# Kernel tuning notes

Measured on AMD Instinct MI355X. Metric: run time of the kernel, lower is better.

## Reference

```python
import jax, jax.numpy as jnp
import numpy as np

TEMPERATURE = 8.0  # sqrt(d_k), d_k = 64


def setup_inputs() -> dict:
    key = jax.random.key(0)
    kq, kk, kv, km = jax.random.split(key, 4)
    B, Lq, Lk, D = 64, 1024, 1024, 64
    q = jax.random.normal(kq, (B, Lq, D), dtype=jnp.float32)
    k = jax.random.normal(kk, (B, Lk, D), dtype=jnp.float32)
    v = jax.random.normal(kv, (B, Lk, D), dtype=jnp.float32)
    mask = jax.random.randint(km, (B, Lq, Lk), 0, 2).astype(jnp.bool_)
    return {"q": q, "k": k, "v": v, "mask": mask}


def reference(q, k, v, mask):
    # attn = q @ k^T / temperature, masked softmax over last dim, then @ v
    attn = jnp.einsum("bqd,bkd->bqk", q, k) / TEMPERATURE
    attn = jnp.where(mask, -jnp.inf, attn)
    attn = jax.nn.softmax(attn, axis=2)
    output = jnp.einsum("bqk,bkd->bqd", attn, v)
    return (output, attn)
```

## Files before the change

kernel.cpp:

```cpp
#include <hip/hip_runtime.h>
#include <hip/hip_bf16.h>


typedef __attribute__((ext_vector_type(8))) short bf16x8;
typedef __attribute__((ext_vector_type(4))) short bf16x4;
typedef __attribute__((ext_vector_type(4))) float f32x4;

#define GLOBAL_AS __attribute__((address_space(1)))
#define LDS_AS    __attribute__((address_space(3)))

static __device__ __forceinline__ short f2bf(float f) {
    return (short)__builtin_bit_cast(unsigned short, __float2bfloat16(f));
}
static __device__ __forceinline__ bf16x8 pack8(float4 a, float4 b) {
    union { bf16x8 v; __hip_bfloat162 h[4]; } u;
    u.h[0] = __float22bfloat162_rn(make_float2(a.x, a.y));
    u.h[1] = __float22bfloat162_rn(make_float2(a.z, a.w));
    u.h[2] = __float22bfloat162_rn(make_float2(b.x, b.y));
    u.h[3] = __float22bfloat162_rn(make_float2(b.z, b.w));
    return u.v;
}
static __device__ __forceinline__ bf16x4 pack4(float a, float b, float c, float d) {
    union { bf16x4 v; __hip_bfloat162 h[2]; } u;
    u.h[0] = __float22bfloat162_rn(make_float2(a, b));
    u.h[1] = __float22bfloat162_rn(make_float2(c, d));
    return u.v;
}

static __device__ __forceinline__ void dma16(void* lds, const void* g) {
    __builtin_amdgcn_global_load_lds((const GLOBAL_AS unsigned*)g,
                                     (LDS_AS unsigned*)lds, 16, 0, 0);
}
static __device__ __forceinline__ void stage8k(short* lds, const short* g, int w, int L) {
    dma16((void*)(lds + (w * 2 + 0) * 512), (const void*)(g + (w * 2 + 0) * 512 + L * 8));
    dma16((void*)(lds + (w * 2 + 1) * 512), (const void*)(g + (w * 2 + 1) * 512 + L * 8));
}

__global__ __launch_bounds__(256) void pre_maskpack(const int* __restrict__ mask,
                                                    unsigned long long* __restrict__ bits) {
    const int L = threadIdx.x & 63;
    long r = ((long)blockIdx.x * 256 + threadIdx.x) >> 6;
    const int* row = mask + r * 1024;
    unsigned long long bl[16];
    #pragma unroll
    for (int kt = 0; kt < 16; ++kt)
        bl[kt] = __ballot(row[kt * 64 + L] != 0);
    unsigned long long x = bl[0];
    #pragma unroll
    for (int j = 1; j < 16; ++j) x = (L == j) ? bl[j] : x;
    if (L < 16) bits[r * 16 + L] = x;
}

__global__ __launch_bounds__(256) void pre_kv(const float* __restrict__ k,
                                              const float* __restrict__ v,
                                              short* __restrict__ kb,
                                              short* __restrict__ vt) {
    __shared__ short t[64][72];
    const int tid = threadIdx.x;
    if (blockIdx.x < 2048) {
        long ci = (long)blockIdx.x * 256 + tid;
        long row = ci >> 3;
        int  c   = (int)(ci & 7);
        const float4* s = (const float4*)(k + row * 64 + c * 8);
        int r = (int)(row & 63);
        short* dst = kb + (row >> 6) * 4096 + (long)r * 64 + ((c ^ (r & 7)) << 3);
        *(bf16x8*)dst = pack8(s[0], s[1]);
    } else {
        const int bkt = blockIdx.x - 2048;
        const int row = tid >> 2;
        const int cg  = (tid & 3) * 16;
        const float* src = v + ((long)bkt * 64 + row) * 64 + cg;
        float4 f0 = ((const float4*)src)[0];
        float4 f1 = ((const float4*)src)[1];
        float4 f2 = ((const float4*)src)[2];
        float4 f3 = ((const float4*)src)[3];
        float vv[16] = {f0.x, f0.y, f0.z, f0.w, f1.x, f1.y, f1.z, f1.w,
                        f2.x, f2.y, f2.z, f2.w, f3.x, f3.y, f3.z, f3.w};
        #pragma unroll
        for (int dd = 0; dd < 16; ++dd) t[cg + dd][row] = f2bf(vv[dd]);
        __syncthreads();
        const int d = tid >> 2, c0 = (tid & 3) * 2;
        short* dstrow = vt + (long)bkt * 4096 + d * 64;
        *(int4*)&dstrow[((c0 ^ (d & 7)) << 3)]       = *(int4*)&t[d][c0 * 8];
        *(int4*)&dstrow[(((c0 + 1) ^ (d & 7)) << 3)] = *(int4*)&t[d][c0 * 8 + 8];
    }
}

__global__ __launch_bounds__(256, 4) void attn_main(
    const float* __restrict__ q, const unsigned long long* __restrict__ bits,
    const short* __restrict__ kb, const short* __restrict__ vt,
    float* __restrict__ out, float* __restrict__ attn)
{
    __shared__ short kbuf[2][4096];
    __shared__ short vbuf[2][4096];
    __shared__ short ptile[4][1024];

    const int tid  = threadIdx.x;
    const int w    = tid >> 6;
    const int L    = tid & 63;
    const int n    = L & 15;
    const int g    = L >> 4;
    const int b    = blockIdx.y;
    const long bq  = (long)b * 1024 + blockIdx.x * 64;

    const short* ktg = kb + (long)b * 65536;
    const short* vtg = vt + (long)b * 65536;

    const float* qrow = q + (bq + 16 * w + n) * 64 + g * 8;
    float4 qa0 = ((const float4*)qrow)[0];
    float4 qa1 = ((const float4*)(qrow + 4))[0];
    float4 qb0 = ((const float4*)(qrow + 32))[0];
    float4 qb1 = ((const float4*)(qrow + 36))[0];
    const float sc = 0.125f * 1.4426950408889634f;
    qa0.x *= sc; qa0.y *= sc; qa0.z *= sc; qa0.w *= sc;
    qa1.x *= sc; qa1.y *= sc; qa1.z *= sc; qa1.w *= sc;
    qb0.x *= sc; qb0.y *= sc; qb0.z *= sc; qb0.w *= sc;
    qb1.x *= sc; qb1.y *= sc; qb1.z *= sc; qb1.w *= sc;
    bf16x8 qf0 = pack8(qa0, qa1);
    bf16x8 qf1 = pack8(qb0, qb1);

    const unsigned long long* mrow_ptr = bits + (bq + 16 * w + n) * 16;
    const int sw = (n & 7);

    float lp = 0.f;
    stage8k(kbuf[0], ktg, w, L);
    __syncthreads();

    for (int kt = 0; kt < 16; ++kt) {
        if (kt < 15) {
            stage8k(kbuf[(kt + 1) & 1], ktg + (kt + 1) * 4096, w, L);
        } else {
            stage8k(kbuf[0], ktg, w, L);
            stage8k(vbuf[0], vtg, w, L);
        }
        unsigned long long mrow = mrow_ptr[kt];
        const short* kl = kbuf[kt & 1];
        f32x4 acc[4];
        #pragma unroll
        for (int t = 0; t < 4; ++t) { acc[t][0]=0.f; acc[t][1]=0.f; acc[t][2]=0.f; acc[t][3]=0.f; }
        #pragma unroll
        for (int t = 0; t < 4; ++t) {
            bf16x8 kf0 = *(const bf16x8*)&kl[(t * 16 + n) * 64 + ((g ^ sw) << 3)];
            bf16x8 kf1 = *(const bf16x8*)&kl[(t * 16 + n) * 64 + (((4 + g) ^ sw) << 3)];
            acc[t] = __builtin_amdgcn_mfma_f32_16x16x32_bf16(kf0, qf0, acc[t], 0, 0, 0);
            acc[t] = __builtin_amdgcn_mfma_f32_16x16x32_bf16(kf1, qf1, acc[t], 0, 0, 0);
        }
        unsigned long long ms = mrow >> (g * 4);
        #pragma unroll
        for (int t = 0; t < 4; ++t)
            #pragma unroll
            for (int i = 0; i < 4; ++i) {
                unsigned bit = (unsigned)(ms >> (t * 16 + i)) & 1u;
                lp += bit ? 0.f : __builtin_exp2f(acc[t][i]);
            }
        __syncthreads();
    }
    float l = lp + __shfl_xor(lp, 16);
    l += __shfl_xor(l, 32);
    const float linv = 1.0f / l;

    f32x4 oacc[4];
    #pragma unroll
    for (int u = 0; u < 4; ++u) { oacc[u][0]=0.f; oacc[u][1]=0.f; oacc[u][2]=0.f; oacc[u][3]=0.f; }

    float* attn_row = attn + (bq + 16 * w + n) * 1024;
    short* pw = ptile[w];

    for (int kt = 0; kt < 16; ++kt) {
        if (kt < 15) {
            stage8k(kbuf[(kt + 1) & 1], ktg + (kt + 1) * 4096, w, L);
            stage8k(vbuf[(kt + 1) & 1], vtg + (kt + 1) * 4096, w, L);
        }
        unsigned long long mrow = mrow_ptr[kt];
        const short* kl = kbuf[kt & 1];
        const short* vl = vbuf[kt & 1];
        f32x4 acc[4];
        #pragma unroll
        for (int t = 0; t < 4; ++t) { acc[t][0]=0.f; acc[t][1]=0.f; acc[t][2]=0.f; acc[t][3]=0.f; }
        #pragma unroll
        for (int t = 0; t < 4; ++t) {
            bf16x8 kf0 = *(const bf16x8*)&kl[(t * 16 + n) * 64 + ((g ^ sw) << 3)];
            bf16x8 kf1 = *(const bf16x8*)&kl[(t * 16 + n) * 64 + (((4 + g) ^ sw) << 3)];
            acc[t] = __builtin_amdgcn_mfma_f32_16x16x32_bf16(kf0, qf0, acc[t], 0, 0, 0);
            acc[t] = __builtin_amdgcn_mfma_f32_16x16x32_bf16(kf1, qf1, acc[t], 0, 0, 0);
        }
        unsigned long long ms = mrow >> (g * 4);
        #pragma unroll
        for (int t = 0; t < 4; ++t) {
            unsigned b0 = (unsigned)(ms >> (t * 16 + 0)) & 1u;
            unsigned b1 = (unsigned)(ms >> (t * 16 + 1)) & 1u;
            unsigned b2 = (unsigned)(ms >> (t * 16 + 2)) & 1u;
            unsigned b3 = (unsigned)(ms >> (t * 16 + 3)) & 1u;
            float p0 = b0 ? 0.f : __builtin_exp2f(acc[t][0]) * linv;
            float p1 = b1 ? 0.f : __builtin_exp2f(acc[t][1]) * linv;
            float p2 = b2 ? 0.f : __builtin_exp2f(acc[t][2]) * linv;
            float p3 = b3 ? 0.f : __builtin_exp2f(acc[t][3]) * linv;
            *(float4*)(attn_row + kt * 64 + t * 16 + g * 4) = make_float4(p0, p1, p2, p3);
            *(bf16x4*)&pw[n * 64 + ((((t * 2) + (g >> 1)) ^ sw) << 3) + (g & 1) * 4] =
                pack4(p0, p1, p2, p3);
        }
        bf16x8 pf0 = *(const bf16x8*)&pw[n * 64 + ((g ^ sw) << 3)];
        bf16x8 pf1 = *(const bf16x8*)&pw[n * 64 + (((4 + g) ^ sw) << 3)];
        #pragma unroll
        for (int u = 0; u < 4; ++u) {
            bf16x8 vf0 = *(const bf16x8*)&vl[(u * 16 + n) * 64 + ((g ^ sw) << 3)];
            bf16x8 vf1 = *(const bf16x8*)&vl[(u * 16 + n) * 64 + (((4 + g) ^ sw) << 3)];
            oacc[u] = __builtin_amdgcn_mfma_f32_16x16x32_bf16(pf0, vf0, oacc[u], 0, 0, 0);
            oacc[u] = __builtin_amdgcn_mfma_f32_16x16x32_bf16(pf1, vf1, oacc[u], 0, 0, 0);
        }
        __syncthreads();
    }

    #pragma unroll
    for (int u = 0; u < 4; ++u)
        #pragma unroll
        for (int i = 0; i < 4; ++i)
            out[(bq + 16 * w + g * 4 + i) * 64 + u * 16 + n] = oacc[u][i];
}

#define KSTRIDE 72
#define PSTRIDE 68
__global__ __launch_bounds__(256) void attn_fallback(
    const float* __restrict__ q, const float* __restrict__ k,
    const float* __restrict__ v, const int* __restrict__ mask,
    float* __restrict__ out, float* __restrict__ attn)
{
    __shared__ unsigned maskbits[64][32];
    __shared__ short kbuf[64 * KSTRIDE];
    __shared__ short vtbuf[64 * KSTRIDE];
    __shared__ float ptilef[4 * 16 * PSTRIDE];

    const int tid  = threadIdx.x;
    const int w    = tid >> 6;
    const int L    = tid & 63;
    const int n    = L & 15;
    const int quad = L >> 4;
    const int b    = blockIdx.y;
    const long bq  = (long)b * 1024 + blockIdx.x * 64;

    const float* qrow = q + (bq + 16 * w + n) * 64 + quad * 8;
    float4 qa0 = ((const float4*)qrow)[0];
    float4 qa1 = ((const float4*)(qrow + 4))[0];
    float4 qb0 = ((const float4*)(qrow + 32))[0];
    float4 qb1 = ((const float4*)(qrow + 36))[0];
    const float sc = 0.125f;
    qa0.x *= sc; qa0.y *= sc; qa0.z *= sc; qa0.w *= sc;
    qa1.x *= sc; qa1.y *= sc; qa1.z *= sc; qa1.w *= sc;
    qb0.x *= sc; qb0.y *= sc; qb0.z *= sc; qb0.w *= sc;
    qb1.x *= sc; qb1.y *= sc; qb1.z *= sc; qb1.w *= sc;
    bf16x8 qf0 = pack8(qa0, qa1);
    bf16x8 qf1 = pack8(qb0, qb1);

    #pragma unroll
    for (int ii = 0; ii < 8; ++ii) {
        int wi  = ii * 256 + tid;
        int row = wi >> 5;
        int wc  = wi & 31;
        const int4* mp = (const int4*)(mask + (bq + row) * 1024 + wc * 32);
        unsigned word = 0;
        #pragma unroll
        for (int j = 0; j < 8; ++j) {
            int4 m4 = mp[j];
            word |= (m4.x != 0 ? 1u : 0u) << (4 * j + 0);
            word |= (m4.y != 0 ? 1u : 0u) << (4 * j + 1);
            word |= (m4.z != 0 ? 1u : 0u) << (4 * j + 2);
            word |= (m4.w != 0 ? 1u : 0u) << (4 * j + 3);
        }
        maskbits[row][wc] = word;
    }

    float m_i[4] = {-1e30f, -1e30f, -1e30f, -1e30f};
    float l_i[4] = {0.f, 0.f, 0.f, 0.f};

    for (int kt = 0; kt < 16; ++kt) {
        __syncthreads();
        {
            const float* kr = k + ((long)b * 1024 + kt * 64 + L) * 64 + w * 16;
            float4 k0 = ((const float4*)kr)[0];
            float4 k1 = ((const float4*)kr)[1];
            float4 k2 = ((const float4*)kr)[2];
            float4 k3 = ((const float4*)kr)[3];
            bf16x8* dst = (bf16x8*)&kbuf[L * KSTRIDE + w * 16];
            dst[0] = pack8(k0, k1);
            dst[1] = pack8(k2, k3);
        }
        __syncthreads();
        f32x4 acc[4];
        #pragma unroll
        for (int t = 0; t < 4; ++t) { acc[t][0]=0.f; acc[t][1]=0.f; acc[t][2]=0.f; acc[t][3]=0.f; }
        #pragma unroll
        for (int t = 0; t < 4; ++t) {
            bf16x8 b0 = *(const bf16x8*)&kbuf[(t * 16 + n) * KSTRIDE + quad * 8];
            bf16x8 b1 = *(const bf16x8*)&kbuf[(t * 16 + n) * KSTRIDE + 32 + quad * 8];
            acc[t] = __builtin_amdgcn_mfma_f32_16x16x32_bf16(qf0, b0, acc[t], 0, 0, 0);
            acc[t] = __builtin_amdgcn_mfma_f32_16x16x32_bf16(qf1, b1, acc[t], 0, 0, 0);
        }
        #pragma unroll
        for (int i = 0; i < 4; ++i) {
            int mrow = 16 * w + quad * 4 + i;
            unsigned w0 = maskbits[mrow][kt * 2];
            unsigned w1 = maskbits[mrow][kt * 2 + 1];
            float s0 = ((w0 >> n)        & 1u) ? -1e30f : acc[0][i];
            float s1 = ((w0 >> (16 + n)) & 1u) ? -1e30f : acc[1][i];
            float s2 = ((w1 >> n)        & 1u) ? -1e30f : acc[2][i];
            float s3 = ((w1 >> (16 + n)) & 1u) ? -1e30f : acc[3][i];
            float mt = fmaxf(fmaxf(s0, s1), fmaxf(s2, s3));
            mt = fmaxf(mt, __shfl_xor(mt, 1));
            mt = fmaxf(mt, __shfl_xor(mt, 2));
            mt = fmaxf(mt, __shfl_xor(mt, 4));
            mt = fmaxf(mt, __shfl_xor(mt, 8));
            float mnew = fmaxf(m_i[i], mt);
            float ps = __expf(s0 - mnew) + __expf(s1 - mnew)
                     + __expf(s2 - mnew) + __expf(s3 - mnew);
            ps += __shfl_xor(ps, 1);
            ps += __shfl_xor(ps, 2);
            ps += __shfl_xor(ps, 4);
            ps += __shfl_xor(ps, 8);
            l_i[i] = l_i[i] * __expf(m_i[i] - mnew) + ps;
            m_i[i] = mnew;
        }
    }
    float linv[4];
    #pragma unroll
    for (int i = 0; i < 4; ++i) linv[i] = 1.0f / l_i[i];

    f32x4 oacc[4];
    #pragma unroll
    for (int t = 0; t < 4; ++t) { oacc[t][0]=0.f; oacc[t][1]=0.f; oacc[t][2]=0.f; oacc[t][3]=0.f; }
    float* attn_row = attn + (bq + 16 * w + n) * 1024;

    for (int kt = 0; kt < 16; ++kt) {
        __syncthreads();
        {
            const float* kr = k + ((long)b * 1024 + kt * 64 + L) * 64 + w * 16;
            float4 k0 = ((const float4*)kr)[0];
            float4 k1 = ((const float4*)kr)[1];
            float4 k2 = ((const float4*)kr)[2];
            float4 k3 = ((const float4*)kr)[3];
            bf16x8* dst = (bf16x8*)&kbuf[L * KSTRIDE + w * 16];
            dst[0] = pack8(k0, k1);
            dst[1] = pack8(k2, k3);
            const float* vr = v + ((long)b * 1024 + kt * 64 + L) * 64 + w * 16;
            float4 v0 = ((const float4*)vr)[0];
            float4 v1 = ((const float4*)vr)[1];
            float4 v2 = ((const float4*)vr)[2];
            float4 v3 = ((const float4*)vr)[3];
            float vv[16] = {v0.x, v0.y, v0.z, v0.w, v1.x, v1.y, v1.z, v1.w,
                            v2.x, v2.y, v2.z, v2.w, v3.x, v3.y, v3.z, v3.w};
            #pragma unroll
            for (int dd = 0; dd < 16; ++dd)
                vtbuf[(w * 16 + dd) * KSTRIDE + L] = f2bf(vv[dd]);
        }
        __syncthreads();
        f32x4 acc[4];
        #pragma unroll
        for (int t = 0; t < 4; ++t) { acc[t][0]=0.f; acc[t][1]=0.f; acc[t][2]=0.f; acc[t][3]=0.f; }
        #pragma unroll
        for (int t = 0; t < 4; ++t) {
            bf16x8 b0 = *(const bf16x8*)&kbuf[(t * 16 + n) * KSTRIDE + quad * 8];
            bf16x8 b1 = *(const bf16x8*)&kbuf[(t * 16 + n) * KSTRIDE + 32 + quad * 8];
            acc[t] = __builtin_amdgcn_mfma_f32_16x16x32_bf16(qf0, b0, acc[t], 0, 0, 0);
            acc[t] = __builtin_amdgcn_mfma_f32_16x16x32_bf16(qf1, b1, acc[t], 0, 0, 0);
        }
        #pragma unroll
        for (int i = 0; i < 4; ++i) {
            int mrow = 16 * w + quad * 4 + i;
            unsigned w0 = maskbits[mrow][kt * 2];
            unsigned w1 = maskbits[mrow][kt * 2 + 1];
            float s0 = ((w0 >> n)        & 1u) ? -1e30f : acc[0][i];
            float s1 = ((w0 >> (16 + n)) & 1u) ? -1e30f : acc[1][i];
            float s2 = ((w1 >> n)        & 1u) ? -1e30f : acc[2][i];
            float s3 = ((w1 >> (16 + n)) & 1u) ? -1e30f : acc[3][i];
            float* pr = &ptilef[(w * 16 + quad * 4 + i) * PSTRIDE];
            pr[n]      = __expf(s0 - m_i[i]) * linv[i];
            pr[16 + n] = __expf(s1 - m_i[i]) * linv[i];
            pr[32 + n] = __expf(s2 - m_i[i]) * linv[i];
            pr[48 + n] = __expf(s3 - m_i[i]) * linv[i];
        }
        bf16x8 pf[2];
        #pragma unroll
        for (int c = 0; c < 2; ++c) {
            const float* pp = &ptilef[(w * 16 + n) * PSTRIDE + c * 32 + quad * 8];
            float4 p0 = ((const float4*)pp)[0];
            float4 p1 = ((const float4*)pp)[1];
            float* ap = attn_row + kt * 64 + c * 32 + quad * 8;
            ((float4*)ap)[0] = p0;
            ((float4*)ap)[1] = p1;
            pf[c] = pack8(p0, p1);
        }
        #pragma unroll
        for (int t = 0; t < 4; ++t) {
            bf16x8 vb0 = *(const bf16x8*)&vtbuf[(t * 16 + n) * KSTRIDE + quad * 8];
            bf16x8 vb1 = *(const bf16x8*)&vtbuf[(t * 16 + n) * KSTRIDE + 32 + quad * 8];
            oacc[t] = __builtin_amdgcn_mfma_f32_16x16x32_bf16(pf[0], vb0, oacc[t], 0, 0, 0);
            oacc[t] = __builtin_amdgcn_mfma_f32_16x16x32_bf16(pf[1], vb1, oacc[t], 0, 0, 0);
        }
    }
    #pragma unroll
    for (int t = 0; t < 4; ++t)
        #pragma unroll
        for (int i = 0; i < 4; ++i)
            out[(bq + 16 * w + quad * 4 + i) * 64 + t * 16 + n] = oacc[t][i];
}

extern "C" void kernel_launch(void* const* d_in, const int* in_sizes, int n_in,
                              void* d_out, int out_size, void* d_ws, size_t ws_size,
                              hipStream_t stream) {
    const float* q    = (const float*)d_in[0];
    const float* k    = (const float*)d_in[1];
    const float* v    = (const float*)d_in[2];
    const int*   mask = (const int*)d_in[3];
    float* out  = (float*)d_out;
    float* attn = out + (long)64 * 1024 * 64;

    dim3 grid(16, 64, 1);
    dim3 block(256, 1, 1);

    const size_t need = (size_t)24 << 20;
    if (ws_size >= need) {
        unsigned char* ws = (unsigned char*)d_ws;
        unsigned long long* bits = (unsigned long long*)ws;
        short* kbw = (short*)(ws + ((size_t)8 << 20));
        short* vtw = (short*)(ws + ((size_t)16 << 20));
        pre_maskpack<<<16384, 256, 0, stream>>>(mask, bits);
        pre_kv<<<3072, 256, 0, stream>>>(k, v, kbw, vtw);
        attn_main<<<grid, block, 0, stream>>>(q, bits, kbw, vtw, out, attn);
    } else {
        attn_fallback<<<grid, block, 0, stream>>>(q, k, v, mask, out, attn);
    }
}
```

Before: 540.9 us.

## Fuse mask bit-packing into attention pass one and add nontemporal loads/stores

Removes the separate pre_maskpack kernel. The first attention pass now reads the int mask directly, packs it into bits per lane, combines them across lanes with shuffles, and writes the packed words to workspace for the second pass to reuse. The grid is also flattened with a remapping that interleaves batches across blocks, and nontemporal loads and stores are used for the streaming K/V conversion, the mask reads, and the attn/out writes. This saves one kernel launch and one extra pass over the mask. In exchange, pass one now does more global loads per lane, and the second pass depends on bits written earlier by the same block without an explicit fence.

```diff
diff --git a/kernel.cpp b/kernel.cpp
--- a/kernel.cpp
+++ b/kernel.cpp
@@ -5,6 +5,7 @@
 typedef __attribute__((ext_vector_type(8))) short bf16x8;
 typedef __attribute__((ext_vector_type(4))) short bf16x4;
 typedef __attribute__((ext_vector_type(4))) float f32x4;
+typedef __attribute__((ext_vector_type(4))) int   i32x4;
 
 #define GLOBAL_AS __attribute__((address_space(1)))
 #define LDS_AS    __attribute__((address_space(3)))
@@ -20,12 +21,23 @@
     u.h[3] = __float22bfloat162_rn(make_float2(b.z, b.w));
     return u.v;
 }
+static __device__ __forceinline__ bf16x8 pack8v(f32x4 a, f32x4 b) {
+    union { bf16x8 v; __hip_bfloat162 h[4]; } u;
+    u.h[0] = __float22bfloat162_rn(make_float2(a[0], a[1]));
+    u.h[1] = __float22bfloat162_rn(make_float2(a[2], a[3]));
+    u.h[2] = __float22bfloat162_rn(make_float2(b[0], b[1]));
+    u.h[3] = __float22bfloat162_rn(make_float2(b[2], b[3]));
+    return u.v;
+}
 static __device__ __forceinline__ bf16x4 pack4(float a, float b, float c, float d) {
     union { bf16x4 v; __hip_bfloat162 h[2]; } u;
     u.h[0] = __float22bfloat162_rn(make_float2(a, b));
     u.h[1] = __float22bfloat162_rn(make_float2(c, d));
     return u.v;
 }
+static __device__ __forceinline__ f32x4 vscale(f32x4 a, float s) {
+    a[0] *= s; a[1] *= s; a[2] *= s; a[3] *= s; return a;
+}
 
 static __device__ __forceinline__ void dma16(void* lds, const void* g) {
     __builtin_amdgcn_global_load_lds((const GLOBAL_AS unsigned*)g,
@@ -34,21 +46,6 @@
 static __device__ __forceinline__ void stage8k(short* lds, const short* g, int w, int L) {
     dma16((void*)(lds + (w * 2 + 0) * 512), (const void*)(g + (w * 2 + 0) * 512 + L * 8));
     dma16((void*)(lds + (w * 2 + 1) * 512), (const void*)(g + (w * 2 + 1) * 512 + L * 8));
-}
-
-__global__ __launch_bounds__(256) void pre_maskpack(const int* __restrict__ mask,
-                                                    unsigned long long* __restrict__ bits) {
-    const int L = threadIdx.x & 63;
-    long r = ((long)blockIdx.x * 256 + threadIdx.x) >> 6;
-    const int* row = mask + r * 1024;
-    unsigned long long bl[16];
-    #pragma unroll
-    for (int kt = 0; kt < 16; ++kt)
-        bl[kt] = __ballot(row[kt * 64 + L] != 0);
-    unsigned long long x = bl[0];
-    #pragma unroll
-    for (int j = 1; j < 16; ++j) x = (L == j) ? bl[j] : x;
-    if (L < 16) bits[r * 16 + L] = x;
 }
 
 __global__ __launch_bounds__(256) void pre_kv(const float* __restrict__ k,
@@ -61,21 +58,23 @@
         long ci = (long)blockIdx.x * 256 + tid;
         long row = ci >> 3;
         int  c   = (int)(ci & 7);
-        const float4* s = (const float4*)(k + row * 64 + c * 8);
+        const f32x4* s = (const f32x4*)(k + row * 64 + c * 8);
+        f32x4 a  = __builtin_nontemporal_load(s);
+        f32x4 b2 = __builtin_nontemporal_load(s + 1);
         int r = (int)(row & 63);
         short* dst = kb + (row >> 6) * 4096 + (long)r * 64 + ((c ^ (r & 7)) << 3);
-        *(bf16x8*)dst = pack8(s[0], s[1]);
+        *(bf16x8*)dst = pack8v(a, b2);
     } else {
         const int bkt = blockIdx.x - 2048;
         const int row = tid >> 2;
         const int cg  = (tid & 3) * 16;
         const float* src = v + ((long)bkt * 64 + row) * 64 + cg;
-        float4 f0 = ((const float4*)src)[0];
-        float4 f1 = ((const float4*)src)[1];
-        float4 f2 = ((const float4*)src)[2];
-        float4 f3 = ((const float4*)src)[3];
-        float vv[16] = {f0.x, f0.y, f0.z, f0.w, f1.x, f1.y, f1.z, f1.w,
-                        f2.x, f2.y, f2.z, f2.w, f3.x, f3.y, f3.z, f3.w};
+        f32x4 f0 = __builtin_nontemporal_load((const f32x4*)src);
+        f32x4 f1 = __builtin_nontemporal_load((const f32x4*)src + 1);
+        f32x4 f2 = __builtin_nontemporal_load((const f32x4*)src + 2);
+        f32x4 f3 = __builtin_nontemporal_load((const f32x4*)src + 3);
+        float vv[16] = {f0[0], f0[1], f0[2], f0[3], f1[0], f1[1], f1[2], f1[3],
+                        f2[0], f2[1], f2[2], f2[3], f3[0], f3[1], f3[2], f3[3]};
         #pragma unroll
         for (int dd = 0; dd < 16; ++dd) t[cg + dd][row] = f2bf(vv[dd]);
         __syncthreads();
@@ -87,7 +86,8 @@
 }
 
 __global__ __launch_bounds__(256, 4) void attn_main(
-    const float* __restrict__ q, const unsigned long long* __restrict__ bits,
+    const float* __restrict__ q, const int* __restrict__ mask,
+    unsigned long long* __restrict__ bits,
     const short* __restrict__ kb, const short* __restrict__ vt,
     float* __restrict__ out, float* __restrict__ attn)
 {
@@ -100,26 +100,28 @@
     const int L    = tid & 63;
     const int n    = L & 15;
     const int g    = L >> 4;
-    const int b    = blockIdx.y;
-    const long bq  = (long)b * 1024 + blockIdx.x * 64;
+    const int lin  = blockIdx.x;
+    const int b    = (lin & 7) * 8 + ((lin >> 3) >> 4);
+    const int qt   = (lin >> 3) & 15;
+    const long bq  = (long)b * 1024 + qt * 64;
 
     const short* ktg = kb + (long)b * 65536;
     const short* vtg = vt + (long)b * 65536;
 
-    const float* qrow = q + (bq + 16 * w + n) * 64 + g * 8;
-    float4 qa0 = ((const float4*)qrow)[0];
-    float4 qa1 = ((const float4*)(qrow + 4))[0];
-    float4 qb0 = ((const float4*)(qrow + 32))[0];
-    float4 qb1 = ((const float4*)(qrow + 36))[0];
+    const long grow = bq + 16 * w + n;
+
+    const float* qrow = q + grow * 64 + g * 8;
+    f32x4 qa0 = ((const f32x4*)qrow)[0];
+    f32x4 qa1 = ((const f32x4*)qrow)[1];
+    f32x4 qb0 = ((const f32x4*)(qrow + 32))[0];
+    f32x4 qb1 = ((const f32x4*)(qrow + 32))[1];
     const float sc = 0.125f * 1.4426950408889634f;
-    qa0.x *= sc; qa0.y *= sc; qa0.z *= sc; qa0.w *= sc;
-    qa1.x *= sc; qa1.y *= sc; qa1.z *= sc; qa1.w *= sc;
-    qb0.x *= sc; qb0.y *= sc; qb0.z *= sc; qb0.w *= sc;
-    qb1.x *= sc; qb1.y *= sc; qb1.z *= sc; qb1.w *= sc;
-    bf16x8 qf0 = pack8(qa0, qa1);
-    bf16x8 qf1 = pack8(qb0, qb1);
-
-    const unsigned long long* mrow_ptr = bits + (bq + 16 * w + n) * 16;
+    qa0 = vscale(qa0, sc); qa1 = vscale(qa1, sc);
+    qb0 = vscale(qb0, sc); qb1 = vscale(qb1, sc);
+    bf16x8 qf0 = pack8v(qa0, qa1);
+    bf16x8 qf1 = pack8v(qb0, qb1);
+
+    const int* mbase = mask + grow * 1024 + g * 4;
     const int sw = (n & 7);
 
     float lp = 0.f;
@@ -133,7 +135,12 @@
             stage8k(kbuf[0], ktg, w, L);
             stage8k(vbuf[0], vtg, w, L);
         }
-        unsigned long long mrow = mrow_ptr[kt];
+        const int* mp = mbase + kt * 64;
+        i32x4 mm0 = __builtin_nontemporal_load((const i32x4*)(mp));
+        i32x4 mm1 = __builtin_nontemporal_load((const i32x4*)(mp + 16));
+        i32x4 mm2 = __builtin_nontemporal_load((const i32x4*)(mp + 32));
+        i32x4 mm3 = __builtin_nontemporal_load((const i32x4*)(mp + 48));
+
         const short* kl = kbuf[kt & 1];
         f32x4 acc[4];
         #pragma unroll
@@ -145,14 +152,24 @@
             acc[t] = __builtin_amdgcn_mfma_f32_16x16x32_bf16(kf0, qf0, acc[t], 0, 0, 0);
             acc[t] = __builtin_amdgcn_mfma_f32_16x16x32_bf16(kf1, qf1, acc[t], 0, 0, 0);
         }
-        unsigned long long ms = mrow >> (g * 4);
+        unsigned nb[4];
+        nb[0] = (mm0[0]!=0?1u:0u)|(mm0[1]!=0?2u:0u)|(mm0[2]!=0?4u:0u)|(mm0[3]!=0?8u:0u);
+        nb[1] = (mm1[0]!=0?1u:0u)|(mm1[1]!=0?2u:0u)|(mm1[2]!=0?4u:0u)|(mm1[3]!=0?8u:0u);
+        nb[2] = (mm2[0]!=0?1u:0u)|(mm2[1]!=0?2u:0u)|(mm2[2]!=0?4u:0u)|(mm2[3]!=0?8u:0u);
+        nb[3] = (mm3[0]!=0?1u:0u)|(mm3[1]!=0?2u:0u)|(mm3[2]!=0?4u:0u)|(mm3[3]!=0?8u:0u);
         #pragma unroll
         for (int t = 0; t < 4; ++t)
             #pragma unroll
-            for (int i = 0; i < 4; ++i) {
-                unsigned bit = (unsigned)(ms >> (t * 16 + i)) & 1u;
-                lp += bit ? 0.f : __builtin_exp2f(acc[t][i]);
-            }
+            for (int i = 0; i < 4; ++i)
+                lp += ((nb[t] >> i) & 1u) ? 0.f : __builtin_exp2f(acc[t][i]);
+        unsigned long long wword =
+              ((unsigned long long)nb[0] << (g * 4))
+            | ((unsigned long long)nb[1] << (16 + g * 4))
+            | ((unsigned long long)nb[2] << (32 + g * 4))
+            | ((unsigned long long)nb[3] << (48 + g * 4));
+        wword |= __shfl_xor(wword, 16);
+        wword |= __shfl_xor(wword, 32);
+        if (g == 0) bits[grow * 16 + kt] = wword;
         __syncthreads();
     }
     float l = lp + __shfl_xor(lp, 16);
@@ -163,7 +180,8 @@
     #pragma unroll
     for (int u = 0; u < 4; ++u) { oacc[u][0]=0.f; oacc[u][1]=0.f; oacc[u][2]=0.f; oacc[u][3]=0.f; }
 
-    float* attn_row = attn + (bq + 16 * w + n) * 1024;
+    const unsigned long long* mrow_ptr = bits + grow * 16;
+    float* attn_row = attn + grow * 1024;
     short* pw = ptile[w];
 
     for (int kt = 0; kt < 16; ++kt) {
@@ -195,7 +213,8 @@
             float p1 = b1 ? 0.f : __builtin_exp2f(acc[t][1]) * linv;
             float p2 = b2 ? 0.f : __builtin_exp2f(acc[t][2]) * linv;
             float p3 = b3 ? 0.f : __builtin_exp2f(acc[t][3]) * linv;
-            *(float4*)(attn_row + kt * 64 + t * 16 + g * 4) = make_float4(p0, p1, p2, p3);
+            f32x4 pv; pv[0] = p0; pv[1] = p1; pv[2] = p2; pv[3] = p3;
+            __builtin_nontemporal_store(pv, (f32x4*)(attn_row + kt * 64 + t * 16 + g * 4));
             *(bf16x4*)&pw[n * 64 + ((((t * 2) + (g >> 1)) ^ sw) << 3) + (g & 1) * 4] =
                 pack4(p0, p1, p2, p3);
         }
@@ -215,7 +234,8 @@
     for (int u = 0; u < 4; ++u)
         #pragma unroll
         for (int i = 0; i < 4; ++i)
-            out[(bq + 16 * w + g * 4 + i) * 64 + u * 16 + n] = oacc[u][i];
+            __builtin_nontemporal_store(oacc[u][i],
+                &out[(bq + 16 * w + g * 4 + i) * 64 + u * 16 + n]);
 }
 
 #define KSTRIDE 72
@@ -413,19 +433,17 @@
     float* out  = (float*)d_out;
     float* attn = out + (long)64 * 1024 * 64;
 
-    dim3 grid(16, 64, 1);
-    dim3 block(256, 1, 1);
-
     const size_t need = (size_t)24 << 20;
     if (ws_size >= need) {
         unsigned char* ws = (unsigned char*)d_ws;
         unsigned long long* bits = (unsigned long long*)ws;
         short* kbw = (short*)(ws + ((size_t)8 << 20));
         short* vtw = (short*)(ws + ((size_t)16 << 20));
-        pre_maskpack<<<16384, 256, 0, stream>>>(mask, bits);
         pre_kv<<<3072, 256, 0, stream>>>(k, v, kbw, vtw);
-        attn_main<<<grid, block, 0, stream>>>(q, bits, kbw, vtw, out, attn);
+        attn_main<<<dim3(1024, 1, 1), dim3(256, 1, 1), 0, stream>>>(
+            q, mask, bits, kbw, vtw, out, attn);
     } else {
-        attn_fallback<<<grid, block, 0, stream>>>(q, k, v, mask, out, attn);
-    }
-}
+        attn_fallback<<<dim3(16, 64, 1), dim3(256, 1, 1), 0, stream>>>(
+            q, k, v, mask, out, attn);
+    }
+}
```

Measured after the change: 538.5 us. About the same (-0.4%).
